# Kernel tuning notes

Measured on AMD Instinct MI355X. Metric: run time of the kernel, lower is better.

## Reference

```python
import jax, jax.numpy as jnp
import numpy as np
import math

D_MODEL = 512
N_HEAD = 8
D_HEAD = 64
N_LAYER = 12
D_FF = 2048
EMB_SIZES = [32, 128, 256, 256, 32, 64]
N_TOKEN = [32, 32, 90, 70, 8, 8]
EPS_ATTN = 1e-6
EPS_LN = 1e-5


def _pos_encoding(seq, d):
    pos = np.arange(seq, dtype=np.float32)[:, None]
    div = np.exp(np.arange(0, d, 2, dtype=np.float32) * (-math.log(10000.0) / d))
    pe = np.zeros((seq, d), np.float32)
    pe[:, 0::2] = np.sin(pos * div)
    pe[:, 1::2] = np.cos(pos * div)
    return jnp.asarray(pe)


def _layernorm(x, g, b):
    mu = jnp.mean(x, axis=-1, keepdims=True)
    var = jnp.var(x, axis=-1, keepdims=True)
    return (x - mu) * jax.lax.rsqrt(var + EPS_LN) * g + b


def _phi(x):
    # elu(x) + 1
    return jnp.where(x > 0, x + 1.0, jnp.exp(x))


def _causal_linear_attention(h, wq, bq, wk, bk, wv, bv, wo, bo):
    B, S, _ = h.shape
    q = _phi((h @ wq + bq).reshape(B, S, N_HEAD, D_HEAD))
    k = _phi((h @ wk + bk).reshape(B, S, N_HEAD, D_HEAD))
    v = (h @ wv + bv).reshape(B, S, N_HEAD, D_HEAD)
    # cumulative K^T V state: [B,S,H,D,D]
    kv = jnp.cumsum(k[..., :, None] * v[..., None, :], axis=1)
    ksum = jnp.cumsum(k, axis=1)
    z = 1.0 / (jnp.einsum('bshd,bshd->bsh', q, ksum) + EPS_ATTN)
    out = jnp.einsum('bshd,bshde->bshe', q, kv) * z[..., None]
    return out.reshape(B, S, D_MODEL) @ wo + bo


def _forward(x, emb_bar, emb_position, emb_pitch, emb_duration, emb_type, emb_emotion,
             in_w, in_b, wq, bq, wk, bk, wv, bv, wo, bo,
             ln1_g, ln1_b, w1, b1, w2, b2, ln2_g, ln2_b,
             lnf_g, lnf_b, proj_emo_w, proj_emo_b):
    tables = [emb_bar, emb_position, emb_pitch, emb_duration, emb_type, emb_emotion]
    embs = jnp.concatenate(
        [jnp.take(t, x[..., i], axis=0) * math.sqrt(EMB_SIZES[i]) for i, t in enumerate(tables)],
        axis=-1)  # [B,S,768]
    h = embs @ in_w + in_b
    S = h.shape[1]
    h = h + _pos_encoding(S, D_MODEL)[None, :, :]  # dropout is identity in eval

    def layer(hc, p):
        (wq_, bq_, wk_, bk_, wv_, bv_, wo_, bo_,
         g1, be1, w1_, b1_, w2_, b2_, g2, be2) = p
        hc = hc + _causal_linear_attention(hc, wq_, bq_, wk_, bk_, wv_, bv_, wo_, bo_)
        hc = _layernorm(hc, g1, be1)
        y = jax.nn.gelu(hc @ w1_ + b1_, approximate=False) @ w2_ + b2_
        hc = _layernorm(hc + y, g2, be2)
        return hc, None

    params = (wq, bq, wk, bk, wv, bv, wo, bo, ln1_g, ln1_b, w1, b1, w2, b2, ln2_g, ln2_b)
    h, _ = jax.lax.scan(layer, h, params)
    h = _layernorm(h, lnf_g, lnf_b)  # final encoder norm
    y_emotion = h @ proj_emo_w + proj_emo_b
    return h, y_emotion


def setup_inputs() -> dict:
    key = jax.random.key(0)
    ks = jax.random.split(key, 16)
    B, S = 1, 1024
    x = jax.random.randint(ks[0], (B, S, 6), 0, 8)

    def lin(k, fin, fout):
        k1, k2 = jax.random.split(k)
        lim = 1.0 / np.sqrt(fin)
        return (jax.random.uniform(k1, (fin, fout), minval=-lim, maxval=lim),
                jax.random.uniform(k2, (fout,), minval=-lim, maxval=lim))

    def stack_lin(k, fin, fout):
        kk = jax.random.split(k, N_LAYER)
        ws, bs = zip(*[lin(kk[i], fin, fout) for i in range(N_LAYER)])
        return jnp.stack(ws), jnp.stack(bs)

    def stack_ln(val):
        return jnp.full((N_LAYER, D_MODEL), val, jnp.float32)

    inp = {'x': x}
    names = ['emb_bar', 'emb_position', 'emb_pitch', 'emb_duration', 'emb_type', 'emb_emotion']
    for i, n in enumerate(names):
        inp[n] = jax.random.normal(jax.random.fold_in(ks[1], i), (N_TOKEN[i], EMB_SIZES[i])) * 0.02
    inp['in_w'], inp['in_b'] = lin(ks[2], sum(EMB_SIZES), D_MODEL)
    inp['wq'], inp['bq'] = stack_lin(ks[3], D_MODEL, D_MODEL)
    inp['wk'], inp['bk'] = stack_lin(ks[4], D_MODEL, D_MODEL)
    inp['wv'], inp['bv'] = stack_lin(ks[5], D_MODEL, D_MODEL)
    inp['wo'], inp['bo'] = stack_lin(ks[6], D_MODEL, D_MODEL)
    inp['ln1_g'], inp['ln1_b'] = stack_ln(1.0), stack_ln(0.0)
    inp['w1'], inp['b1'] = stack_lin(ks[7], D_MODEL, D_FF)
    inp['w2'], inp['b2'] = stack_lin(ks[8], D_FF, D_MODEL)
    inp['ln2_g'], inp['ln2_b'] = stack_ln(1.0), stack_ln(0.0)
    inp['lnf_g'], inp['lnf_b'] = jnp.ones((D_MODEL,)), jnp.zeros((D_MODEL,))
    inp['proj_emo_w'], inp['proj_emo_b'] = lin(ks[9], D_MODEL, N_TOKEN[5])
    return inp


def reference(x, emb_bar, emb_position, emb_pitch, emb_duration, emb_type, emb_emotion,
              in_w, in_b, wq, bq, wk, bk, wv, bv, wo, bo,
              ln1_g, ln1_b, w1, b1, w2, b2, ln2_g, ln2_b,
              lnf_g, lnf_b, proj_emo_w, proj_emo_b):
    return _forward(x, emb_bar, emb_position, emb_pitch, emb_duration, emb_type, emb_emotion,
                    in_w, in_b, wq, bq, wk, bk, wv, bv, wo, bo,
                    ln1_g, ln1_b, w1, b1, w2, b2, ln2_g, ln2_b,
                    lnf_g, lnf_b, proj_emo_w, proj_emo_b)
```

## Files before the change

### kernel.cpp

```cpp
#include <hip/hip_runtime.h>
#include <hip/hip_bf16.h>
#include <math.h>


#define S_LEN 1024
#define DM 512
#define NH 8
#define DH 64
#define DFF 2048
#define NLAYER 12
#define CHUNK 64
#define NCH (S_LEN / CHUNK)

#define ACT_NONE 0
#define ACT_PHI  1
#define ACT_GELU 2

typedef short s16x8 __attribute__((ext_vector_type(8)));
typedef float f32x4 __attribute__((ext_vector_type(4)));

__device__ __forceinline__ short f2bf(float x) {
    __hip_bfloat16 h = __float2bfloat16(x);
    return *reinterpret_cast<short*>(&h);
}

__device__ __forceinline__ void fma4(f32x4& a, float s, const f32x4 v) {
    a.x = fmaf(s, v.x, a.x); a.y = fmaf(s, v.y, a.y);
    a.z = fmaf(s, v.z, a.z); a.w = fmaf(s, v.w, a.w);
}

__global__ __launch_bounds__(256) void embed_kernel(
    const int* __restrict__ x,
    const float* __restrict__ t0, const float* __restrict__ t1,
    const float* __restrict__ t2, const float* __restrict__ t3,
    const float* __restrict__ t4, const float* __restrict__ t5,
    short* __restrict__ EMBb)
{
    int s = blockIdx.x;
    __shared__ int xi[6];
    if (threadIdx.x < 6) xi[threadIdx.x] = x[s * 6 + threadIdx.x];
    __syncthreads();
    for (int j = threadIdx.x; j < 768; j += 256) {
        int i, off, width; const float* t; float sc;
        if (j < 32)       { i = 0; off = 0;   t = t0; sc = 5.656854249f;  width = 32;  }
        else if (j < 160) { i = 1; off = 32;  t = t1; sc = 11.3137085f;   width = 128; }
        else if (j < 416) { i = 2; off = 160; t = t2; sc = 16.0f;         width = 256; }
        else if (j < 672) { i = 3; off = 416; t = t3; sc = 16.0f;         width = 256; }
        else if (j < 704) { i = 4; off = 672; t = t4; sc = 5.656854249f;  width = 32;  }
        else              { i = 5; off = 704; t = t5; sc = 8.0f;          width = 64;  }
        EMBb[s * 768 + j] = f2bf(t[xi[i] * width + (j - off)] * sc);
    }
}

__global__ __launch_bounds__(256) void transpose_w(
    const float* __restrict__ in, short* __restrict__ out, int K, int N)
{
    __shared__ short t[64][66];
    const int b = blockIdx.z;
    const int n0 = blockIdx.x * 64, k0 = blockIdx.y * 64;
    const float* ip = in + (size_t)b * K * N;
    short* op = out + (size_t)b * K * N;
    const int c = threadIdx.x & 63, r0 = (threadIdx.x >> 6) * 16;
    #pragma unroll
    for (int i = 0; i < 16; ++i)
        t[c][r0 + i] = f2bf(ip[(size_t)(k0 + r0 + i) * N + n0 + c]);
    __syncthreads();
    #pragma unroll
    for (int i = 0; i < 16; ++i)
        op[(size_t)(n0 + r0 + i) * K + k0 + c] = t[r0 + i][c];
}

__device__ __forceinline__ float apply_act(float v, int act) {
    if (act == ACT_PHI)       return (v > 0.0f) ? (v + 1.0f) : expf(v);
    else if (act == ACT_GELU) return 0.5f * v * (1.0f + erff(v * 0.70710678118654752f));
    return v;
}


__device__ __forceinline__ void ldswr64(short* lds, int srow, int scolb,
                                        const s16x8 r[2])
{
    const int bc = scolb ^ ((srow & 7) << 4);
    #pragma unroll
    for (int p = 0; p < 2; ++p)
        *(s16x8*)((char*)lds + (p * 32 + srow) * 128 + bc) = r[p];
}

__device__ __forceinline__ void compute64(
    const short* __restrict__ As, const short* __restrict__ Bs,
    int wr, int wc, int l15, int q, f32x4 acc[2][2])
{
    #pragma unroll
    for (int kh = 0; kh < 2; ++kh) {
        const int kb = kh * 64 + q * 16;
        s16x8 a[2], b[2];
        #pragma unroll
        for (int m = 0; m < 2; ++m) {
            int row = wr * 32 + m * 16 + l15;
            a[m] = *(const s16x8*)((const char*)As + row * 128 + (kb ^ ((row & 7) << 4)));
        }
        #pragma unroll
        for (int n = 0; n < 2; ++n) {
            int row = wc * 32 + n * 16 + l15;
            b[n] = *(const s16x8*)((const char*)Bs + row * 128 + (kb ^ ((row & 7) << 4)));
        }
        #pragma unroll
        for (int m = 0; m < 2; ++m)
            #pragma unroll
            for (int n = 0; n < 2; ++n)
                acc[m][n] = __builtin_amdgcn_mfma_f32_16x16x32_bf16(
                    a[m], b[n], acc[m][n], 0, 0, 0);
    }
}

__global__ __launch_bounds__(256) void gemm64(
    const short* __restrict__ A, const short* __restrict__ BT,
    const float* __restrict__ bias, const float* __restrict__ resid,
    float* __restrict__ Cf, short* __restrict__ Cbf,
    int N, int K, int act, int add_pe)
{
    __shared__ short As[2][4096];
    __shared__ short Bs[2][4096];
    const int tid = threadIdx.x;
    const int row0 = blockIdx.y * 64, col0 = blockIdx.x * 64;
    const int w = tid >> 6, lane = tid & 63, q = lane >> 4, l15 = lane & 15;
    const int wr = w >> 1, wc = w & 1;
    const int nt = K >> 6;

    const int srow = tid >> 3;
    const int scolb = (tid & 7) * 16;
    const char* gA = (const char*)(A  + (size_t)(row0 + srow) * K) + scolb;
    const char* gB = (const char*)(BT + (size_t)(col0 + srow) * K) + scolb;
    const size_t rstep = (size_t)32 * K * 2;

    s16x8 ra[2], rb[2];
    #pragma unroll
    for (int p = 0; p < 2; ++p) {
        ra[p] = *(const s16x8*)(gA + p * rstep);
        rb[p] = *(const s16x8*)(gB + p * rstep);
    }
    ldswr64(As[0], srow, scolb, ra);
    ldswr64(Bs[0], srow, scolb, rb);
    if (nt > 1) {
        #pragma unroll
        for (int p = 0; p < 2; ++p) {
            ra[p] = *(const s16x8*)(gA + p * rstep + 128);
            rb[p] = *(const s16x8*)(gB + p * rstep + 128);
        }
    }
    __syncthreads();

    f32x4 acc[2][2] = {};
    int cur = 0;
    for (int t = 0; t < nt; ++t) {
        if (t + 1 < nt) {
            ldswr64(As[cur ^ 1], srow, scolb, ra);
            ldswr64(Bs[cur ^ 1], srow, scolb, rb);
        }
        if (t + 2 < nt) {
            size_t ko = (size_t)(t + 2) * 128;
            #pragma unroll
            for (int p = 0; p < 2; ++p) {
                ra[p] = *(const s16x8*)(gA + p * rstep + ko);
                rb[p] = *(const s16x8*)(gB + p * rstep + ko);
            }
        }
        compute64(As[cur], Bs[cur], wr, wc, l15, q, acc);
        __syncthreads();
        cur ^= 1;
    }

    const int rbase = row0 + wr * 32 + q * 4;
    const int cbase = col0 + wc * 32 + l15;
    #pragma unroll
    for (int n = 0; n < 2; ++n) {
        int c = cbase + n * 16;
        float bia = bias[c];
        #pragma unroll
        for (int m = 0; m < 2; ++m) {
            #pragma unroll
            for (int rg = 0; rg < 4; ++rg) {
                int r = rbase + m * 16 + rg;
                float v = apply_act(acc[m][n][rg] + bia, act);
                if (resid) v += resid[(size_t)r * N + c];
                if (add_pe) {
                    float freq = expf((float)(c & ~1) * (-9.210340371976184f / 512.0f));
                    float ang = (float)r * freq;
                    v += (c & 1) ? cosf(ang) : sinf(ang);
                }
                if (Cf)  Cf[(size_t)r * N + c] = v;
                if (Cbf) Cbf[(size_t)r * N + c] = f2bf(v);
            }
        }
    }
}

__global__ __launch_bounds__(256) void qkv64(
    const short* __restrict__ Hb,
    const short* __restrict__ qT, const short* __restrict__ kT, const short* __restrict__ vT,
    const float* __restrict__ bq, const float* __restrict__ bk, const float* __restrict__ bv,
    float* __restrict__ Qb, float* __restrict__ Kb, float* __restrict__ Vb)
{
    __shared__ short As[2][4096];
    __shared__ short Bs[2][4096];
    const int sel  = blockIdx.x >> 3;
    const int col0 = (blockIdx.x & 7) * 64;
    const int row0 = blockIdx.y * 64;
    const short* BT   = (sel == 0) ? qT : (sel == 1) ? kT : vT;
    const float* bias = (sel == 0) ? bq : (sel == 1) ? bk : bv;
    float* C          = (sel == 0) ? Qb : (sel == 1) ? Kb : Vb;
    const bool phi = (sel < 2);

    const int tid = threadIdx.x;
    const int w = tid >> 6, lane = tid & 63, q = lane >> 4, l15 = lane & 15;
    const int wr = w >> 1, wc = w & 1;

    const int srow = tid >> 3;
    const int scolb = (tid & 7) * 16;
    const char* gA = (const char*)(Hb + (size_t)(row0 + srow) * DM) + scolb;
    const char* gB = (const char*)(BT + (size_t)(col0 + srow) * DM) + scolb;
    const size_t rstep = (size_t)32 * DM * 2;

    s16x8 ra[2], rb[2];
    #pragma unroll
    for (int p = 0; p < 2; ++p) {
        ra[p] = *(const s16x8*)(gA + p * rstep);
        rb[p] = *(const s16x8*)(gB + p * rstep);
    }
    ldswr64(As[0], srow, scolb, ra);
    ldswr64(Bs[0], srow, scolb, rb);
    #pragma unroll
    for (int p = 0; p < 2; ++p) {
        ra[p] = *(const s16x8*)(gA + p * rstep + 128);
        rb[p] = *(const s16x8*)(gB + p * rstep + 128);
    }
    __syncthreads();

    f32x4 acc[2][2] = {};
    int cur = 0;
    for (int t = 0; t < 8; ++t) {
        if (t + 1 < 8) {
            ldswr64(As[cur ^ 1], srow, scolb, ra);
            ldswr64(Bs[cur ^ 1], srow, scolb, rb);
        }
        if (t + 2 < 8) {
            size_t ko = (size_t)(t + 2) * 128;
            #pragma unroll
            for (int p = 0; p < 2; ++p) {
                ra[p] = *(const s16x8*)(gA + p * rstep + ko);
                rb[p] = *(const s16x8*)(gB + p * rstep + ko);
            }
        }
        compute64(As[cur], Bs[cur], wr, wc, l15, q, acc);
        __syncthreads();
        cur ^= 1;
    }

    const int rbase = row0 + wr * 32 + q * 4;
    const int cbase = col0 + wc * 32 + l15;
    #pragma unroll
    for (int n = 0; n < 2; ++n) {
        int c = cbase + n * 16;
        float bia = bias[c];
        #pragma unroll
        for (int m = 0; m < 2; ++m) {
            #pragma unroll
            for (int rg = 0; rg < 4; ++rg) {
                int r = rbase + m * 16 + rg;
                float v = acc[m][n][rg] + bia;
                if (phi) v = (v > 0.0f) ? (v + 1.0f) : expf(v);
                C[(size_t)r * DM + c] = v;
            }
        }
    }
}

__global__ __launch_bounds__(256) void chunk_stats_kernel(
    const float* __restrict__ Kb, const float* __restrict__ Vb,
    float* __restrict__ KVC, float* __restrict__ KSC)
{
    const int h = blockIdx.x >> 4, c = blockIdx.x & 15;
    const int tid = threadIdx.x;
    __shared__ float Ks[64][68];
    __shared__ float Vs[64][68];
    #pragma unroll
    for (int it = 0; it < 4; ++it) {
        int j = tid + it * 256;
        int r = j >> 4, d0 = (j & 15) * 4;
        size_t g = (size_t)(c * CHUNK + r) * DM + h * 64 + d0;
        *(f32x4*)(&Ks[r][d0]) = *(const f32x4*)(Kb + g);
        *(f32x4*)(&Vs[r][d0]) = *(const f32x4*)(Vb + g);
    }
    __syncthreads();
    const int di = (tid >> 4) * 4, ei = (tid & 15) * 4;
    f32x4 a0 = {}, a1 = {}, a2 = {}, a3 = {}, ks = {};
    #pragma unroll 8
    for (int t = 0; t < 64; ++t) {
        f32x4 kk = *(const f32x4*)(&Ks[t][di]);
        f32x4 vv = *(const f32x4*)(&Vs[t][ei]);
        fma4(a0, kk.x, vv); fma4(a1, kk.y, vv);
        fma4(a2, kk.z, vv); fma4(a3, kk.w, vv);
        ks += kk;
    }
    float* out = KVC + (size_t)(c * NH + h) * 4096;
    *(f32x4*)(out + (size_t)(di + 0) * 64 + ei) = a0;
    *(f32x4*)(out + (size_t)(di + 1) * 64 + ei) = a1;
    *(f32x4*)(out + (size_t)(di + 2) * 64 + ei) = a2;
    *(f32x4*)(out + (size_t)(di + 3) * 64 + ei) = a3;
    if ((tid & 15) == 0)
        *(f32x4*)(KSC + (size_t)(c * NH + h) * 64 + di) = ks;
}

__global__ __launch_bounds__(256) void scan_kv_kernel(
    float* __restrict__ KVC, float* __restrict__ KSC)
{
    int gid = blockIdx.x * 256 + threadIdx.x;
    int h = gid >> 10, e4 = gid & 1023;
    f32x4* p = (f32x4*)KVC;
    f32x4 run = {};
    #pragma unroll
    for (int c = 0; c < NCH; ++c) {
        size_t idx = (size_t)(c * NH + h) * 1024 + e4;
        f32x4 v = p[idx];
        p[idx] = run;
        run += v;
    }
    if (gid < NH * 64) {
        int h2 = gid >> 6, e = gid & 63;
        float r = 0.0f;
        for (int c = 0; c < NCH; ++c) {
            size_t idx = (size_t)(c * NH + h2) * 64 + e;
            float v = KSC[idx];
            KSC[idx] = r;
            r += v;
        }
    }
}

__global__ __launch_bounds__(256) void attn_out_kernel(
    const float* __restrict__ Qb, const float* __restrict__ Kb,
    const float* __restrict__ Vb, const float* __restrict__ KVC,
    const float* __restrict__ KSC, short* __restrict__ Ab)
{
    const int h = blockIdx.x >> 4, c = blockIdx.x & 15;
    const int tid = threadIdx.x;
    __shared__ float Qt[64][68];
    __shared__ float Kt[64][68];
    __shared__ float Vs[64][68];
    __shared__ float Ms[64][68];
    __shared__ float St[64][68];
    __shared__ float KSs[64];

    const float* ms_src = KVC + (size_t)(c * NH + h) * 4096;
    #pragma unroll
    for (int it = 0; it < 4; ++it) {
        int j = tid + it * 256;
        int r = j >> 4, d0 = (j & 15) * 4;
        size_t g = (size_t)(c * CHUNK + r) * DM + h * 64 + d0;
        f32x4 q = *(const f32x4*)(Qb + g);
        f32x4 k = *(const f32x4*)(Kb + g);
        f32x4 v = *(const f32x4*)(Vb + g);
        Qt[d0 + 0][r] = q.x; Qt[d0 + 1][r] = q.y; Qt[d0 + 2][r] = q.z; Qt[d0 + 3][r] = q.w;
        Kt[d0 + 0][r] = k.x; Kt[d0 + 1][r] = k.y; Kt[d0 + 2][r] = k.z; Kt[d0 + 3][r] = k.w;
        *(f32x4*)(&Vs[r][d0]) = v;
        *(f32x4*)(&Ms[r][d0]) = *(const f32x4*)(ms_src + (size_t)j * 4);
    }
    if (tid < 64) KSs[tid] = KSC[(size_t)(c * NH + h) * 64 + tid];
    __syncthreads();

    const int si = tid >> 4, ti = tid & 15;
    const int s0 = si * 4, t0 = ti * 4;

    f32x4 accO0 = {}, accO1 = {}, accO2 = {}, accO3 = {};
    f32x4 den = {};
    #pragma unroll 8
    for (int d = 0; d < 64; ++d) {
        f32x4 qv = *(const f32x4*)(&Qt[d][s0]);
        f32x4 mv = *(const f32x4*)(&Ms[d][t0]);
        float ks = KSs[d];
        fma4(accO0, qv.x, mv); fma4(accO1, qv.y, mv);
        fma4(accO2, qv.z, mv); fma4(accO3, qv.w, mv);
        fma4(den, ks, qv);
    }

    f32x4 p0 = {}, p1 = {}, p2 = {}, p3 = {};
    if (ti <= si) {
        #pragma unroll 8
        for (int d = 0; d < 64; ++d) {
            f32x4 qv = *(const f32x4*)(&Qt[d][s0]);
            f32x4 kv = *(const f32x4*)(&Kt[d][t0]);
            fma4(p0, qv.x, kv); fma4(p1, qv.y, kv);
            fma4(p2, qv.z, kv); fma4(p3, qv.w, kv);
        }
        if (ti == si) {
            p0.y = 0.0f; p0.z = 0.0f; p0.w = 0.0f;
            p1.z = 0.0f; p1.w = 0.0f;
            p2.w = 0.0f;
        }
    }
    St[t0 + 0][s0 + 0] = p0.x; St[t0 + 1][s0 + 0] = p0.y;
    St[t0 + 2][s0 + 0] = p0.z; St[t0 + 3][s0 + 0] = p0.w;
    St[t0 + 0][s0 + 1] = p1.x; St[t0 + 1][s0 + 1] = p1.y;
    St[t0 + 2][s0 + 1] = p1.z; St[t0 + 3][s0 + 1] = p1.w;
    St[t0 + 0][s0 + 2] = p2.x; St[t0 + 1][s0 + 2] = p2.y;
    St[t0 + 2][s0 + 2] = p2.z; St[t0 + 3][s0 + 2] = p2.w;
    St[t0 + 0][s0 + 3] = p3.x; St[t0 + 1][s0 + 3] = p3.y;
    St[t0 + 2][s0 + 3] = p3.z; St[t0 + 3][s0 + 3] = p3.w;
    __syncthreads();

    const int tmax = s0 + 4;
    #pragma unroll 4
    for (int t2 = 0; t2 < tmax; ++t2) {
        f32x4 sv = *(const f32x4*)(&St[t2][s0]);
        f32x4 vv = *(const f32x4*)(&Vs[t2][t0]);
        fma4(accO0, sv.x, vv); fma4(accO1, sv.y, vv);
        fma4(accO2, sv.z, vv); fma4(accO3, sv.w, vv);
        den += sv;
    }

    short* op = Ab + (size_t)(c * CHUNK + s0) * DM + h * 64 + t0;
    {
        float z = 1.0f / (den.x + 1e-6f);
        short4 o; o.x = f2bf(accO0.x * z); o.y = f2bf(accO0.y * z);
        o.z = f2bf(accO0.z * z); o.w = f2bf(accO0.w * z);
        *reinterpret_cast<short4*>(op) = o;
    }
    {
        float z = 1.0f / (den.y + 1e-6f);
        short4 o; o.x = f2bf(accO1.x * z); o.y = f2bf(accO1.y * z);
        o.z = f2bf(accO1.z * z); o.w = f2bf(accO1.w * z);
        *reinterpret_cast<short4*>(op + DM) = o;
    }
    {
        float z = 1.0f / (den.z + 1e-6f);
        short4 o; o.x = f2bf(accO2.x * z); o.y = f2bf(accO2.y * z);
        o.z = f2bf(accO2.z * z); o.w = f2bf(accO2.w * z);
        *reinterpret_cast<short4*>(op + 2 * DM) = o;
    }
    {
        float z = 1.0f / (den.w + 1e-6f);
        short4 o; o.x = f2bf(accO3.x * z); o.y = f2bf(accO3.y * z);
        o.z = f2bf(accO3.z * z); o.w = f2bf(accO3.w * z);
        *reinterpret_cast<short4*>(op + 3 * DM) = o;
    }
}

__device__ __forceinline__ float block_reduce_sum(float v, float* smem)
{
    #pragma unroll
    for (int o = 32; o > 0; o >>= 1) v += __shfl_down(v, o, 64);
    int w = threadIdx.x >> 6;
    if ((threadIdx.x & 63) == 0) smem[w] = v;
    __syncthreads();
    v = smem[0] + smem[1] + smem[2] + smem[3];
    __syncthreads();
    return v;
}

__global__ __launch_bounds__(256) void ln_kernel(
    const float* __restrict__ X, const float* __restrict__ g,
    const float* __restrict__ b, float* __restrict__ O, short* __restrict__ Ob)
{
    __shared__ float red[4];
    const int row = blockIdx.x;
    const float* x = X + (size_t)row * DM;
    const int t = threadIdx.x;
    float v0 = x[t], v1 = x[t + 256];
    float mean = block_reduce_sum(v0 + v1, red) * (1.0f / 512.0f);
    float d0 = v0 - mean, d1 = v1 - mean;
    float var = block_reduce_sum(d0 * d0 + d1 * d1, red) * (1.0f / 512.0f);
    float rs = 1.0f / sqrtf(var + 1e-5f);
    float o0 = d0 * rs * g[t] + b[t];
    float o1 = d1 * rs * g[t + 256] + b[t + 256];
    O[(size_t)row * DM + t]       = o0;
    O[(size_t)row * DM + t + 256] = o1;
    if (Ob) {
        Ob[(size_t)row * DM + t]       = f2bf(o0);
        Ob[(size_t)row * DM + t + 256] = f2bf(o1);
    }
}

__global__ __launch_bounds__(256) void proj_emo_kernel(
    const float* __restrict__ HF, const float* __restrict__ pw,
    const float* __restrict__ pb, float* __restrict__ out)
{
    int idx = blockIdx.x * 256 + threadIdx.x;
    int r = idx >> 3, e = idx & 7;
    float acc = pb[e];
    const float* h = HF + (size_t)r * DM;
    for (int d = 0; d < DM; ++d) acc += h[d] * pw[d * 8 + e];
    out[idx] = acc;
}

extern "C" void kernel_launch(void* const* d_in, const int* in_sizes, int n_in,
                              void* d_out, int out_size, void* d_ws, size_t ws_size,
                              hipStream_t stream)
{
    const int*   x    = (const int*)d_in[0];
    const float* e0   = (const float*)d_in[1];
    const float* e1   = (const float*)d_in[2];
    const float* e2   = (const float*)d_in[3];
    const float* e3   = (const float*)d_in[4];
    const float* e4   = (const float*)d_in[5];
    const float* e5   = (const float*)d_in[6];
    const float* in_w = (const float*)d_in[7];
    const float* in_b = (const float*)d_in[8];
    const float* wq   = (const float*)d_in[9];
    const float* bq   = (const float*)d_in[10];
    const float* wk   = (const float*)d_in[11];
    const float* bk   = (const float*)d_in[12];
    const float* wv   = (const float*)d_in[13];
    const float* bv   = (const float*)d_in[14];
    const float* wo   = (const float*)d_in[15];
    const float* bo   = (const float*)d_in[16];
    const float* g1   = (const float*)d_in[17];
    const float* be1  = (const float*)d_in[18];
    const float* w1   = (const float*)d_in[19];
    const float* b1   = (const float*)d_in[20];
    const float* w2   = (const float*)d_in[21];
    const float* b2   = (const float*)d_in[22];
    const float* g2   = (const float*)d_in[23];
    const float* be2  = (const float*)d_in[24];
    const float* gf   = (const float*)d_in[25];
    const float* bfin = (const float*)d_in[26];
    const float* pw   = (const float*)d_in[27];
    const float* pb   = (const float*)d_in[28];
    float* outp = (float*)d_out;

    float* ws = (float*)d_ws;
    float* H    = ws;
    float* Y    = ws + 524288;
    float* Qb   = ws + 1048576;
    float* Kb   = ws + 1572864;
    float* Vb   = ws + 2097152;
    float* KVC  = ws + 2621440;
    float* KSC  = ws + 3145728;
    short* sb   = (short*)(ws + 3153920);
    short* Hb   = sb;
    short* Ab   = sb + 524288;
    short* FFb  = sb + 1048576;
    short* EMBb = FFb;
    short* inT  = sb + 3145728;
    short* qT   = inT + 393216;
    short* kT   = qT + 3145728;
    short* vT   = kT + 3145728;
    short* oT   = vT + 3145728;
    short* w1T  = oT + 3145728;
    short* w2T  = w1T + 12582912;

    const dim3 blk256(256);

    transpose_w<<<dim3(8, 12, 1),  blk256, 0, stream>>>(in_w, inT, 768, DM);
    transpose_w<<<dim3(8, 8, 12),  blk256, 0, stream>>>(wq, qT, DM, DM);
    transpose_w<<<dim3(8, 8, 12),  blk256, 0, stream>>>(wk, kT, DM, DM);
    transpose_w<<<dim3(8, 8, 12),  blk256, 0, stream>>>(wv, vT, DM, DM);
    transpose_w<<<dim3(8, 8, 12),  blk256, 0, stream>>>(wo, oT, DM, DM);
    transpose_w<<<dim3(32, 8, 12), blk256, 0, stream>>>(w1, w1T, DM, DFF);
    transpose_w<<<dim3(8, 32, 12), blk256, 0, stream>>>(w2, w2T, DFF, DM);

    embed_kernel<<<S_LEN, blk256, 0, stream>>>(x, e0, e1, e2, e3, e4, e5, EMBb);
    gemm64<<<dim3(8, 16), blk256, 0, stream>>>(EMBb, inT, in_b, nullptr,
                                               H, Hb, DM, 768, ACT_NONE, 1);

    for (int l = 0; l < NLAYER; ++l) {
        const short* qT_l = qT + (size_t)l * DM * DM;
        const short* kT_l = kT + (size_t)l * DM * DM;
        const short* vT_l = vT + (size_t)l * DM * DM;
        const short* oT_l = oT + (size_t)l * DM * DM;
        const short* w1T_l = w1T + (size_t)l * DM * DFF;
        const short* w2T_l = w2T + (size_t)l * DM * DFF;
        const float* bq_l = bq + l * DM;  const float* bk_l = bk + l * DM;
        const float* bv_l = bv + l * DM;  const float* bo_l = bo + l * DM;
        const float* b1_l = b1 + l * DFF; const float* b2_l = b2 + l * DM;

        qkv64<<<dim3(24, 16), blk256, 0, stream>>>(Hb, qT_l, kT_l, vT_l,
                                                   bq_l, bk_l, bv_l, Qb, Kb, Vb);

        chunk_stats_kernel<<<NCH * NH, blk256, 0, stream>>>(Kb, Vb, KVC, KSC);
        scan_kv_kernel<<<32, blk256, 0, stream>>>(KVC, KSC);
        attn_out_kernel<<<NCH * NH, blk256, 0, stream>>>(Qb, Kb, Vb, KVC, KSC, Ab);

        gemm64<<<dim3(8, 16), blk256, 0, stream>>>(Ab, oT_l, bo_l, H,
                                                   Y, nullptr, DM, DM, ACT_NONE, 0);
        ln_kernel<<<S_LEN, blk256, 0, stream>>>(Y, g1 + l * DM, be1 + l * DM, H, Hb);

        gemm64<<<dim3(32, 16), blk256, 0, stream>>>(Hb, w1T_l, b1_l, nullptr,
                                                    nullptr, FFb, DFF, DM, ACT_GELU, 0);
        gemm64<<<dim3(8, 16), blk256, 0, stream>>>(FFb, w2T_l, b2_l, H,
                                                   Y, nullptr, DM, DFF, ACT_NONE, 0);
        ln_kernel<<<S_LEN, blk256, 0, stream>>>(Y, g2 + l * DM, be2 + l * DM, H, Hb);
    }

    ln_kernel<<<S_LEN, blk256, 0, stream>>>(H, gf, bfin, outp, nullptr);
    proj_emo_kernel<<<8192 / 256, blk256, 0, stream>>>(outp, pw, pb, outp + 524288);
}
```

Before: 1.179 ms.

## Split-K the FFN down-projection, fold KV scan into attention, cache projection weights

The second FFN GEMM (K=2048) is now split into two K halves across blockIdx.z, which doubles its grid from 128 to 256 blocks. The two partial outputs and the residual are summed inside the following layernorm. The separate scan kernel is removed, and each attention-output block now sums the preceding chunks' KV states itself. That cuts a launch per layer but adds redundant reads that grow with chunk index. The emotion projection also stages its weights in shared memory and loads hidden rows as vectors. Together these trade some extra memory traffic for better GPU occupancy and fewer launches.

Result: faster. 1.112 ms (-5.8%).

```diff
diff --git a/kernel.cpp b/kernel.cpp
--- a/kernel.cpp
+++ b/kernel.cpp
@@ -117,20 +117,23 @@
     const short* __restrict__ A, const short* __restrict__ BT,
     const float* __restrict__ bias, const float* __restrict__ resid,
     float* __restrict__ Cf, short* __restrict__ Cbf,
-    int N, int K, int act, int add_pe)
+    int N, int K, int act, int add_pe, int zparts)
 {
     __shared__ short As[2][4096];
     __shared__ short Bs[2][4096];
     const int tid = threadIdx.x;
     const int row0 = blockIdx.y * 64, col0 = blockIdx.x * 64;
+    const int z = blockIdx.z;
+    const int Kz = K / zparts;
+    const int kbase = z * Kz;
     const int w = tid >> 6, lane = tid & 63, q = lane >> 4, l15 = lane & 15;
     const int wr = w >> 1, wc = w & 1;
-    const int nt = K >> 6;
+    const int nt = Kz >> 6;
 
     const int srow = tid >> 3;
     const int scolb = (tid & 7) * 16;
-    const char* gA = (const char*)(A  + (size_t)(row0 + srow) * K) + scolb;
-    const char* gB = (const char*)(BT + (size_t)(col0 + srow) * K) + scolb;
+    const char* gA = (const char*)(A  + (size_t)(row0 + srow) * K + kbase) + scolb;
+    const char* gB = (const char*)(BT + (size_t)(col0 + srow) * K + kbase) + scolb;
     const size_t rstep = (size_t)32 * K * 2;
 
     s16x8 ra[2], rb[2];
@@ -170,12 +173,14 @@
         cur ^= 1;
     }
 
+    if (zparts > 1 && Cf) Cf += (size_t)z * S_LEN * N;
+
     const int rbase = row0 + wr * 32 + q * 4;
     const int cbase = col0 + wc * 32 + l15;
     #pragma unroll
     for (int n = 0; n < 2; ++n) {
         int c = cbase + n * 16;
-        float bia = bias[c];
+        float bia = (z == 0) ? bias[c] : 0.0f;
         #pragma unroll
         for (int m = 0; m < 2; ++m) {
             #pragma unroll
@@ -311,32 +316,6 @@
         *(f32x4*)(KSC + (size_t)(c * NH + h) * 64 + di) = ks;
 }
 
-__global__ __launch_bounds__(256) void scan_kv_kernel(
-    float* __restrict__ KVC, float* __restrict__ KSC)
-{
-    int gid = blockIdx.x * 256 + threadIdx.x;
-    int h = gid >> 10, e4 = gid & 1023;
-    f32x4* p = (f32x4*)KVC;
-    f32x4 run = {};
-    #pragma unroll
-    for (int c = 0; c < NCH; ++c) {
-        size_t idx = (size_t)(c * NH + h) * 1024 + e4;
-        f32x4 v = p[idx];
-        p[idx] = run;
-        run += v;
-    }
-    if (gid < NH * 64) {
-        int h2 = gid >> 6, e = gid & 63;
-        float r = 0.0f;
-        for (int c = 0; c < NCH; ++c) {
-            size_t idx = (size_t)(c * NH + h2) * 64 + e;
-            float v = KSC[idx];
-            KSC[idx] = r;
-            r += v;
-        }
-    }
-}
-
 __global__ __launch_bounds__(256) void attn_out_kernel(
     const float* __restrict__ Qb, const float* __restrict__ Kb,
     const float* __restrict__ Vb, const float* __restrict__ KVC,
@@ -351,7 +330,26 @@
     __shared__ float St[64][68];
     __shared__ float KSs[64];
 
-    const float* ms_src = KVC + (size_t)(c * NH + h) * 4096;
+    {
+        f32x4 macc[4] = {};
+        for (int cp = 0; cp < c; ++cp) {
+            const float* src = KVC + (size_t)(cp * NH + h) * 4096;
+            #pragma unroll
+            for (int it = 0; it < 4; ++it)
+                macc[it] += *(const f32x4*)(src + (size_t)(tid + it * 256) * 4);
+        }
+        #pragma unroll
+        for (int it = 0; it < 4; ++it) {
+            int j = tid + it * 256;
+            *(f32x4*)(&Ms[j >> 4][(j & 15) * 4]) = macc[it];
+        }
+        if (tid < 64) {
+            float s = 0.0f;
+            for (int cp = 0; cp < c; ++cp)
+                s += KSC[(size_t)(cp * NH + h) * 64 + tid];
+            KSs[tid] = s;
+        }
+    }
     #pragma unroll
     for (int it = 0; it < 4; ++it) {
         int j = tid + it * 256;
@@ -363,9 +361,7 @@
         Qt[d0 + 0][r] = q.x; Qt[d0 + 1][r] = q.y; Qt[d0 + 2][r] = q.z; Qt[d0 + 3][r] = q.w;
         Kt[d0 + 0][r] = k.x; Kt[d0 + 1][r] = k.y; Kt[d0 + 2][r] = k.z; Kt[d0 + 3][r] = k.w;
         *(f32x4*)(&Vs[r][d0]) = v;
-        *(f32x4*)(&Ms[r][d0]) = *(const f32x4*)(ms_src + (size_t)j * 4);
-    }
-    if (tid < 64) KSs[tid] = KSC[(size_t)(c * NH + h) * 64 + tid];
+    }
     __syncthreads();
 
     const int si = tid >> 4, ti = tid & 15;
@@ -458,25 +454,29 @@
 }
 
 __global__ __launch_bounds__(256) void ln_kernel(
-    const float* __restrict__ X, const float* __restrict__ g,
-    const float* __restrict__ b, float* __restrict__ O, short* __restrict__ Ob)
+    const float* __restrict__ X, const float* __restrict__ X2,
+    const float* __restrict__ resid,
+    const float* __restrict__ g, const float* __restrict__ b,
+    float* __restrict__ O, short* __restrict__ Ob)
 {
     __shared__ float red[4];
     const int row = blockIdx.x;
-    const float* x = X + (size_t)row * DM;
+    const size_t base = (size_t)row * DM;
     const int t = threadIdx.x;
-    float v0 = x[t], v1 = x[t + 256];
+    float v0 = X[base + t], v1 = X[base + t + 256];
+    if (X2)    { v0 += X2[base + t];    v1 += X2[base + t + 256]; }
+    if (resid) { v0 += resid[base + t]; v1 += resid[base + t + 256]; }
     float mean = block_reduce_sum(v0 + v1, red) * (1.0f / 512.0f);
     float d0 = v0 - mean, d1 = v1 - mean;
     float var = block_reduce_sum(d0 * d0 + d1 * d1, red) * (1.0f / 512.0f);
     float rs = 1.0f / sqrtf(var + 1e-5f);
     float o0 = d0 * rs * g[t] + b[t];
     float o1 = d1 * rs * g[t + 256] + b[t + 256];
-    O[(size_t)row * DM + t]       = o0;
-    O[(size_t)row * DM + t + 256] = o1;
+    O[base + t]       = o0;
+    O[base + t + 256] = o1;
     if (Ob) {
-        Ob[(size_t)row * DM + t]       = f2bf(o0);
-        Ob[(size_t)row * DM + t + 256] = f2bf(o1);
+        Ob[base + t]       = f2bf(o0);
+        Ob[base + t + 256] = f2bf(o1);
     }
 }
 
@@ -484,11 +484,18 @@
     const float* __restrict__ HF, const float* __restrict__ pw,
     const float* __restrict__ pb, float* __restrict__ out)
 {
+    __shared__ float pws[4096];
+    for (int i = threadIdx.x; i < 4096; i += 256) pws[i] = pw[i];
+    __syncthreads();
     int idx = blockIdx.x * 256 + threadIdx.x;
     int r = idx >> 3, e = idx & 7;
     float acc = pb[e];
     const float* h = HF + (size_t)r * DM;
-    for (int d = 0; d < DM; ++d) acc += h[d] * pw[d * 8 + e];
+    for (int d = 0; d < DM; d += 4) {
+        f32x4 hv = *(const f32x4*)(h + d);
+        acc += hv.x * pws[(d + 0) * 8 + e] + hv.y * pws[(d + 1) * 8 + e]
+             + hv.z * pws[(d + 2) * 8 + e] + hv.w * pws[(d + 3) * 8 + e];
+    }
     out[idx] = acc;
 }
 
@@ -530,12 +537,13 @@
     float* ws = (float*)d_ws;
     float* H    = ws;
     float* Y    = ws + 524288;
-    float* Qb   = ws + 1048576;
-    float* Kb   = ws + 1572864;
-    float* Vb   = ws + 2097152;
-    float* KVC  = ws + 2621440;
-    float* KSC  = ws + 3145728;
-    short* sb   = (short*)(ws + 3153920);
+    float* Y2   = ws + 1048576;
+    float* Qb   = ws + 1572864;
+    float* Kb   = ws + 2097152;
+    float* Vb   = ws + 2621440;
+    float* KVC  = ws + 3145728;
+    float* KSC  = ws + 3670016;
+    short* sb   = (short*)(ws + 3678208);
     short* Hb   = sb;
     short* Ab   = sb + 524288;
     short* FFb  = sb + 1048576;
@@ -559,8 +567,8 @@
     transpose_w<<<dim3(8, 32, 12), blk256, 0, stream>>>(w2, w2T, DFF, DM);
 
     embed_kernel<<<S_LEN, blk256, 0, stream>>>(x, e0, e1, e2, e3, e4, e5, EMBb);
-    gemm64<<<dim3(8, 16), blk256, 0, stream>>>(EMBb, inT, in_b, nullptr,
-                                               H, Hb, DM, 768, ACT_NONE, 1);
+    gemm64<<<dim3(8, 16, 1), blk256, 0, stream>>>(EMBb, inT, in_b, nullptr,
+                                                  H, Hb, DM, 768, ACT_NONE, 1, 1);
 
     for (int l = 0; l < NLAYER; ++l) {
         const short* qT_l = qT + (size_t)l * DM * DM;
@@ -577,20 +585,21 @@
                                                    bq_l, bk_l, bv_l, Qb, Kb, Vb);
 
         chunk_stats_kernel<<<NCH * NH, blk256, 0, stream>>>(Kb, Vb, KVC, KSC);
-        scan_kv_kernel<<<32, blk256, 0, stream>>>(KVC, KSC);
         attn_out_kernel<<<NCH * NH, blk256, 0, stream>>>(Qb, Kb, Vb, KVC, KSC, Ab);
 
-        gemm64<<<dim3(8, 16), blk256, 0, stream>>>(Ab, oT_l, bo_l, H,
-                                                   Y, nullptr, DM, DM, ACT_NONE, 0);
-        ln_kernel<<<S_LEN, blk256, 0, stream>>>(Y, g1 + l * DM, be1 + l * DM, H, Hb);
-
-        gemm64<<<dim3(32, 16), blk256, 0, stream>>>(Hb, w1T_l, b1_l, nullptr,
-                                                    nullptr, FFb, DFF, DM, ACT_GELU, 0);
-        gemm64<<<dim3(8, 16), blk256, 0, stream>>>(FFb, w2T_l, b2_l, H,
-                                                   Y, nullptr, DM, DFF, ACT_NONE, 0);
-        ln_kernel<<<S_LEN, blk256, 0, stream>>>(Y, g2 + l * DM, be2 + l * DM, H, Hb);
-    }
-
-    ln_kernel<<<S_LEN, blk256, 0, stream>>>(H, gf, bfin, outp, nullptr);
+        gemm64<<<dim3(8, 16, 1), blk256, 0, stream>>>(Ab, oT_l, bo_l, H,
+                                                      Y, nullptr, DM, DM, ACT_NONE, 0, 1);
+        ln_kernel<<<S_LEN, blk256, 0, stream>>>(Y, nullptr, nullptr,
+                                                g1 + l * DM, be1 + l * DM, H, Hb);
+
+        gemm64<<<dim3(32, 16, 1), blk256, 0, stream>>>(Hb, w1T_l, b1_l, nullptr,
+                                                       nullptr, FFb, DFF, DM, ACT_GELU, 0, 1);
+        gemm64<<<dim3(8, 16, 2), blk256, 0, stream>>>(FFb, w2T_l, b2_l, nullptr,
+                                                      Y, nullptr, DM, DFF, ACT_NONE, 0, 2);
+        ln_kernel<<<S_LEN, blk256, 0, stream>>>(Y, Y2, H,
+                                                g2 + l * DM, be2 + l * DM, H, Hb);
+    }
+
+    ln_kernel<<<S_LEN, blk256, 0, stream>>>(H, nullptr, nullptr, gf, bfin, outp, nullptr);
     proj_emo_kernel<<<8192 / 256, blk256, 0, stream>>>(outp, pw, pb, outp + 524288);
 }
```
